# Optimization experiments

Measured on AMD Instinct MI355X. Metric: run time of the kernel, lower is better.

The kernel has to match this reference:

```python
import jax, jax.numpy as jnp
import numpy as np

IN_DIM = 64
OUT_DIM = 64
NUM_HEADS = 4
NEG_SLOPE = 0.2
GAMMA = 1.0  # constraint_gamma
NUM_VARS = 100000
NUM_CLAUSES = 100000
NUM_CLUSTERS = 2048
VARS_PER = 64
CLAUSES_PER = 64
NUM_EDGES = 400000


def _xavier(k, shape):
    bound = np.sqrt(6.0 / (shape[0] + shape[1])).astype(np.float32)
    return jax.random.uniform(k, shape, jnp.float32, -bound, bound)


def setup_inputs() -> dict:
    key = jax.random.key(0)
    ks = jax.random.split(key, 11)
    return {
        "x_var": jax.random.normal(ks[0], (NUM_VARS, IN_DIM), jnp.float32),
        "x_clause": jax.random.normal(ks[1], (NUM_CLAUSES, IN_DIM), jnp.float32),
        "var_clause_edge_index": jax.random.randint(ks[2], (2, NUM_EDGES), 0, NUM_VARS),
        "edge_polarity": jax.random.normal(ks[3], (NUM_EDGES, 1), jnp.float32),
        "cluster_var_ids": jax.random.randint(ks[4], (NUM_CLUSTERS, VARS_PER), 0, NUM_VARS),
        "cluster_clause_ids": jax.random.randint(ks[5], (NUM_CLUSTERS, CLAUSES_PER), 0, NUM_CLAUSES),
        "satisfaction_scores": jax.random.uniform(ks[6], (NUM_CLAUSES,), jnp.float32),
        "active_heads": 4,
        "W_Q": _xavier(ks[7], (OUT_DIM, IN_DIM)),
        "W_K": _xavier(ks[8], (OUT_DIM, IN_DIM)),
        "W_V": _xavier(ks[9], (OUT_DIM, IN_DIM)),
        "head_weights": jnp.ones((NUM_HEADS,), jnp.float32),
        "out_proj_w": _xavier(ks[10], (OUT_DIM, OUT_DIM)),
        "out_proj_b": jnp.zeros((OUT_DIM,), jnp.float32),
    }


def reference(x_var, x_clause, var_clause_edge_index, edge_polarity,
              cluster_var_ids, cluster_clause_ids, satisfaction_scores,
              active_heads, W_Q, W_K, W_V, head_weights, out_proj_w, out_proj_b):
    # NOTE: var_clause_edge_index / edge_polarity are accepted but unused,
    # matching the original forward body.
    num_vars = x_var.shape[0]
    x_all = jnp.concatenate([x_var, x_clause], axis=0)            # [N, D]
    Q = x_all @ W_Q.T
    K = x_all @ W_K.T
    V = x_all @ W_V.T

    # Block-diagonal cluster layout: [C, S] with S = VARS_PER + CLAUSES_PER
    nodes = jnp.concatenate([cluster_var_ids, cluster_clause_ids + num_vars], axis=1)
    Qc = Q[nodes]                                                 # [C, S, D]
    Kc = K[nodes]
    Vc = V[nodes]

    scale = jnp.asarray(np.sqrt(OUT_DIM), Qc.dtype)
    scores = jnp.einsum('csd,ctd->cst', Qc, Kc) / scale            # [C, S, S]
    # constraint-aware bias on clause columns (added before leaky_relu)
    bias = jnp.concatenate(
        [jnp.zeros(cluster_var_ids.shape, scores.dtype),
         GAMMA * satisfaction_scores[cluster_clause_ids]], axis=1)  # [C, S]
    scores = jax.nn.leaky_relu(scores + bias[:, None, :], NEG_SLOPE)
    attn = jax.nn.softmax(scores, axis=-1)

    head_w = jnp.mean(head_weights[:active_heads])
    h = jnp.einsum('cst,ctd->csd', attn, Vc) * head_w             # [C, S, D]

    flat = nodes.reshape(-1)
    out = jnp.zeros_like(x_all).at[flat].add(h.reshape(-1, OUT_DIM))
    count = jnp.zeros((x_all.shape[0],), x_all.dtype).at[flat].add(1.0)
    out = out / jnp.maximum(count, 1.0)[:, None]
    out = out @ out_proj_w.T + out_proj_b

    return (x_var + out[:num_vars], x_clause + out[num_vars:])
```

## Files before the change

kernel.cpp:

```cpp
#include <hip/hip_runtime.h>


#define NV 100000
#define NN 200000
#define NCLUST 2048
#define XS 72

typedef __attribute__((ext_vector_type(8))) short short8;
typedef __attribute__((ext_vector_type(16))) float floatx16;
typedef __attribute__((ext_vector_type(4))) unsigned uint4v;

__device__ __forceinline__ unsigned short f2bf(float f) {
    union { float f; unsigned u; } v; v.f = f;
    unsigned r = v.u + 0x7fffu + ((v.u >> 16) & 1u);
    return (unsigned short)(r >> 16);
}
__device__ __forceinline__ unsigned pack2bf(float lo, float hi) {
    union { float f; unsigned u; } a, b; a.f = lo; b.f = hi;
    unsigned ra = a.u + 0x7fffu + ((a.u >> 16) & 1u);
    unsigned rb = b.u + 0x7fffu + ((b.u >> 16) & 1u);
    return (ra >> 16) | (rb & 0xffff0000u);
}
__device__ __forceinline__ int crow(int r, int lane) {
    return (r & 3) + 8 * (r >> 2) + 4 * (lane >> 5);
}
__device__ __forceinline__ void bar_lds() {
    __builtin_amdgcn_sched_barrier(0);
    asm volatile("s_waitcnt lgkmcnt(0)" ::: "memory");
    __builtin_amdgcn_s_barrier();
    __builtin_amdgcn_sched_barrier(0);
}

#define ZU4 1650000
__global__ __launch_bounds__(256) void prep_kernel(
    const float* __restrict__ WQ, const float* __restrict__ WK,
    const float* __restrict__ WV, const float* __restrict__ Wout,
    const float* __restrict__ head_weights, const int* __restrict__ active_heads_p,
    unsigned short* __restrict__ Mtr, unsigned short* __restrict__ Pbf,
    uint4v* __restrict__ zbase)
{
    int o = blockIdx.x * blockDim.x + threadIdx.x;
    if (o < 4096) {
        int d = o >> 6, a = o & 63;
        float acc = 0.f;
        for (int j = 0; j < 64; ++j) acc += WQ[j*64 + a] * WK[j*64 + d];
        Mtr[o] = f2bf(acc * 0.125f);
    } else if (o < 8192) {
        int ah = active_heads_p[0];
        float hw = 0.f;
        for (int i = 0; i < ah; ++i) hw += head_weights[i];
        hw /= (float)ah;
        int o2 = o - 4096;
        int j = o2 >> 6, b = o2 & 63;
        float acc = 0.f;
        for (int d = 0; d < 64; ++d) acc += Wout[j*64 + d] * WV[d*64 + b];
        Pbf[o2] = f2bf(acc * hw);
    }
    uint4v z = {0u, 0u, 0u, 0u};
    for (int j = o; j < ZU4; j += 262144) zbase[j] = z;
}

template<bool WN>
__device__ __forceinline__ void cluster_compute(
    unsigned short* X, unsigned short* E,
    const int* ids, const float* biascl,
    const unsigned short* __restrict__ Mtr,
    unsigned short* __restrict__ accum_bf,
    int lane, int w, int m, int hk, int r, int cb,
    short8 nx0, short8 nx1, short8 nx2, short8 nx3)
{
    {
        floatx16 z0 = {}, z1 = {};
        #pragma unroll
        for (int ks = 0; ks < 4; ++ks) {
            short8 mb0 = *(const short8*)(Mtr + m * 64 + ks * 16 + hk);
            short8 mb1 = *(const short8*)(Mtr + (32 + m) * 64 + ks * 16 + hk);
            short8 a = *(const short8*)&X[(w * 32 + m) * XS + ks * 16 + hk];
            z0 = __builtin_amdgcn_mfma_f32_32x32x16_bf16(a, mb0, z0, 0, 0, 0);
            z1 = __builtin_amdgcn_mfma_f32_32x32x16_bf16(a, mb1, z1, 0, 0, 0);
        }
        #pragma unroll
        for (int rr = 0; rr < 16; ++rr) {
            int row = w * 32 + crow(rr, lane);
            E[row * XS + m]      = f2bf(z0[rr]);
            E[row * XS + 32 + m] = f2bf(z1[rr]);
        }
    }

    floatx16 sc[4] = {{}, {}, {}, {}};
    #pragma unroll
    for (int ks = 0; ks < 4; ++ks) {
        short8 a = *(const short8*)&E[(w * 32 + m) * XS + ks * 16 + hk];
        #pragma unroll
        for (int nt = 0; nt < 4; ++nt) {
            short8 b = *(const short8*)&X[(nt * 32 + m) * XS + ks * 16 + hk];
            sc[nt] = __builtin_amdgcn_mfma_f32_32x32x16_bf16(a, b, sc[nt], 0, 0, 0);
        }
    }

    const float b2 = biascl[m], b3 = biascl[32 + m];
    #pragma unroll
    for (int rr = 0; rr < 16; ++rr) {
        float a0 = sc[0][rr], a1 = sc[1][rr], a2 = sc[2][rr] + b2, a3 = sc[3][rr] + b3;
        a0 = a0 > 0.f ? a0 : 0.2f * a0;
        a1 = a1 > 0.f ? a1 : 0.2f * a1;
        a2 = a2 > 0.f ? a2 : 0.2f * a2;
        a3 = a3 > 0.f ? a3 : 0.2f * a3;
        a0 = __expf(a0); a1 = __expf(a1); a2 = __expf(a2); a3 = __expf(a3);
        float s4 = (a0 + a1) + (a2 + a3);
        #pragma unroll
        for (int off = 1; off < 32; off <<= 1) s4 += __shfl_xor(s4, off, 64);
        float inv = __builtin_amdgcn_rcpf(s4);
        sc[0][rr] = a0 * inv; sc[1][rr] = a1 * inv;
        sc[2][rr] = a2 * inv; sc[3][rr] = a3 * inv;
    }

    #pragma unroll
    for (int rr = 0; rr < 16; ++rr) {
        int row = w * 32 + crow(rr, lane);
        E[row * XS + m]      = f2bf(sc[0][rr]);
        E[row * XS + 32 + m] = f2bf(sc[1][rr]);
    }

    floatx16 g0 = {}, g1 = {};
    #pragma unroll
    for (int ks = 0; ks < 4; ++ks) {
        short8 a = *(const short8*)&E[(w * 32 + m) * XS + ks * 16 + hk];
        short8 b0, b1;
        #pragma unroll
        for (int j = 0; j < 8; ++j) {
            int t = ks * 16 + hk + j;
            b0[j] = (short)X[t * XS + m];
            b1[j] = (short)X[t * XS + 32 + m];
        }
        g0 = __builtin_amdgcn_mfma_f32_32x32x16_bf16(a, b0, g0, 0, 0, 0);
        g1 = __builtin_amdgcn_mfma_f32_32x32x16_bf16(a, b1, g1, 0, 0, 0);
    }

    #pragma unroll
    for (int rr = 0; rr < 16; ++rr) {
        int row = w * 32 + crow(rr, lane);
        E[row * XS + m]      = f2bf(sc[2][rr]);
        E[row * XS + 32 + m] = f2bf(sc[3][rr]);
    }

    #pragma unroll
    for (int ks = 0; ks < 4; ++ks) {
        short8 a = *(const short8*)&E[(w * 32 + m) * XS + ks * 16 + hk];
        short8 b0, b1;
        #pragma unroll
        for (int j = 0; j < 8; ++j) {
            int t = 64 + ks * 16 + hk + j;
            b0[j] = (short)X[t * XS + m];
            b1[j] = (short)X[t * XS + 32 + m];
        }
        g0 = __builtin_amdgcn_mfma_f32_32x32x16_bf16(a, b0, g0, 0, 0, 0);
        g1 = __builtin_amdgcn_mfma_f32_32x32x16_bf16(a, b1, g1, 0, 0, 0);
    }

    if (WN) {
        *(short8*)&E[r * XS + cb +  0] = nx0;
        *(short8*)&E[r * XS + cb +  8] = nx1;
        *(short8*)&E[r * XS + cb + 16] = nx2;
        *(short8*)&E[r * XS + cb + 24] = nx3;
    }

    const bool ev = !(lane & 1);
    const int colbase = ev ? m : (31 + m);
    #pragma unroll
    for (int rr = 0; rr < 16; ++rr) {
        int row = w * 32 + crow(rr, lane);
        int nid = ids[row];
        float a0 = g0[rr], a1 = g1[rr];
        float t0 = __shfl_xor(a0, 1, 64);
        float t1 = __shfl_xor(a1, 1, 64);
        float lo = ev ? a0 : t1;
        float hi = ev ? t0 : a1;
        unsigned pk = (unsigned)f2bf(lo) | ((unsigned)f2bf(hi) << 16);
        unsigned long long addr =
            (unsigned long long)(accum_bf + (size_t)nid * 64 + colbase);
        asm volatile("global_atomic_pk_add_bf16 %0, %1, off"
                     :: "v"(addr), "v"(pk) : "memory");
    }
}

__global__ __launch_bounds__(256, 4) void attn_kernel(
    const float* __restrict__ x_var, const float* __restrict__ x_clause,
    const int* __restrict__ cvar, const int* __restrict__ ccl,
    const float* __restrict__ sat, const unsigned short* __restrict__ Mtr,
    unsigned short* __restrict__ accum_bf, float* __restrict__ countv)
{
    __shared__ unsigned short bufA[128 * XS];
    __shared__ unsigned short bufB[128 * XS];
    __shared__ int   ids0[128], ids1[128];
    __shared__ float bias0[64], bias1[64];

    const int tid = threadIdx.x, lane = tid & 63, w = tid >> 6;
    const int m = lane & 31, hk = (lane >> 5) * 8;
    const int c0 = blockIdx.x * 2;
    const int r = tid >> 1, half = tid & 1, cb = half * 32;

    int nid0, nid1;
    const float *src0, *src1;
    float sv0 = 0.f, sv1 = 0.f;
    if (r < 64) {
        nid0 = cvar[c0 * 64 + r];
        nid1 = cvar[c0 * 64 + 64 + r];
        src0 = x_var + (size_t)nid0 * 64;
        src1 = x_var + (size_t)nid1 * 64;
    } else {
        int cid0 = ccl[c0 * 64 + (r - 64)];
        int cid1 = ccl[c0 * 64 + r];
        nid0 = NV + cid0; nid1 = NV + cid1;
        src0 = x_clause + (size_t)cid0 * 64;
        src1 = x_clause + (size_t)cid1 * 64;
        if (half) { sv0 = sat[cid0]; sv1 = sat[cid1]; }
    }

    const float4* s40 = (const float4*)src0 + half * 8;
    const float4* s41 = (const float4*)src1 + half * 8;
    float4 v0[8], v1[8];
    #pragma unroll
    for (int i = 0; i < 8; ++i) v0[i] = s40[i];
    #pragma unroll
    for (int i = 0; i < 8; ++i) v1[i] = s41[i];

    if (!half) {
        ids0[r] = nid0; ids1[r] = nid1;
        atomicAdd(&countv[nid0], 1.0f);
        atomicAdd(&countv[nid1], 1.0f);
    }
    if (r >= 64 && half) { bias0[r - 64] = sv0; bias1[r - 64] = sv1; }

    {
        union { unsigned u[16]; short8 v[4]; } h0;
        #pragma unroll
        for (int i = 0; i < 8; ++i) {
            h0.u[2*i]   = pack2bf(v0[i].x, v0[i].y);
            h0.u[2*i+1] = pack2bf(v0[i].z, v0[i].w);
        }
        #pragma unroll
        for (int i = 0; i < 4; ++i) *(short8*)&bufA[r * XS + cb + i * 8] = h0.v[i];
    }
    union { unsigned u[16]; short8 v[4]; } h1;
    #pragma unroll
    for (int i = 0; i < 8; ++i) {
        h1.u[2*i]   = pack2bf(v1[i].x, v1[i].y);
        h1.u[2*i+1] = pack2bf(v1[i].z, v1[i].w);
    }

    bar_lds();

    cluster_compute<true>(bufA, bufB, ids0, bias0, Mtr, accum_bf,
                          lane, w, m, hk, r, cb,
                          h1.v[0], h1.v[1], h1.v[2], h1.v[3]);

    bar_lds();

    short8 zz = {};
    cluster_compute<false>(bufB, bufA, ids1, bias1, Mtr, accum_bf,
                           lane, w, m, hk, r, cb, zz, zz, zz, zz);
}

__global__ __launch_bounds__(256, 4) void finalize_kernel(
    const float* __restrict__ x_var, const float* __restrict__ x_clause,
    const unsigned short* __restrict__ accum_bf, const float* __restrict__ countv,
    const unsigned short* __restrict__ Pbf, const float* __restrict__ bout,
    float* __restrict__ out)
{
    __shared__ float T[4][32][68];
    __shared__ float cnts[256];
    const int tid = threadIdx.x, lane = tid & 63, w = tid >> 6;
    const int base = blockIdx.x * 256;
    {
        int n = base + tid;
        cnts[tid] = (n < NN) ? countv[n] : 1.f;
    }
    __syncthreads();

    const int m = lane & 31, hk = (lane >> 5) * 8;
    short8 pb[2][4];
    #pragma unroll
    for (int nt = 0; nt < 2; ++nt)
        #pragma unroll
        for (int ks = 0; ks < 4; ++ks)
            pb[nt][ks] = *(const short8*)(Pbf + (nt * 32 + m) * 64 + ks * 16 + hk);
    const float bias0 = bout[m], bias1 = bout[32 + m];

    const int r2 = lane >> 1, cb2 = (lane & 1) * 32;

    #pragma unroll
    for (int tm = 0; tm < 2; ++tm) {
        int mt = w * 2 + tm;
        const unsigned short* arow = accum_bf + (size_t)(base + mt * 32 + m) * 64;
        floatx16 c0 = {}, c1 = {};
        #pragma unroll
        for (int ks = 0; ks < 4; ++ks) {
            short8 a = *(const short8*)(arow + ks * 16 + hk);
            c0 = __builtin_amdgcn_mfma_f32_32x32x16_bf16(a, pb[0][ks], c0, 0, 0, 0);
            c1 = __builtin_amdgcn_mfma_f32_32x32x16_bf16(a, pb[1][ks], c1, 0, 0, 0);
        }
        #pragma unroll
        for (int rr = 0; rr < 16; ++rr) {
            int lr32 = crow(rr, lane);
            float inv = 1.0f / fmaxf(cnts[mt * 32 + lr32], 1.0f);
            T[w][lr32][m]      = c0[rr] * inv + bias0;
            T[w][lr32][32 + m] = c1[rr] * inv + bias1;
        }
        int n2 = base + mt * 32 + r2;
        if (n2 < NN) {
            const float* xr = (n2 < NV) ? (x_var + (size_t)n2 * 64)
                                        : (x_clause + (size_t)(n2 - NV) * 64);
            float* orow = out + (size_t)n2 * 64;
            #pragma unroll
            for (int j = 0; j < 8; ++j) {
                float4 t = *(const float4*)&T[w][r2][cb2 + 4 * j];
                float4 xv = *(const float4*)&xr[cb2 + 4 * j];
                float4 o;
                o.x = t.x + xv.x; o.y = t.y + xv.y;
                o.z = t.z + xv.z; o.w = t.w + xv.w;
                *(float4*)&orow[cb2 + 4 * j] = o;
            }
        }
    }
}

extern "C" void kernel_launch(void* const* d_in, const int* in_sizes, int n_in,
                              void* d_out, int out_size, void* d_ws, size_t ws_size,
                              hipStream_t stream)
{
    const float* x_var        = (const float*)d_in[0];
    const float* x_clause     = (const float*)d_in[1];
    const int*   cvar         = (const int*)d_in[4];
    const int*   ccl          = (const int*)d_in[5];
    const float* sat          = (const float*)d_in[6];
    const int*   active_heads = (const int*)d_in[7];
    const float* WQ           = (const float*)d_in[8];
    const float* WK           = (const float*)d_in[9];
    const float* WV           = (const float*)d_in[10];
    const float* head_weights = (const float*)d_in[11];
    const float* Wout         = (const float*)d_in[12];
    const float* bout         = (const float*)d_in[13];

    unsigned short* accum_bf = (unsigned short*)d_ws;
    float* countv = (float*)(accum_bf + (size_t)NN * 64);
    unsigned short* Mtr = (unsigned short*)(countv + NN);
    unsigned short* Pbf = Mtr + 4096;

    prep_kernel<<<1024, 256, 0, stream>>>(WQ, WK, WV, Wout, head_weights,
                                          active_heads, Mtr, Pbf,
                                          (uint4v*)d_ws);
    attn_kernel<<<NCLUST / 2, 256, 0, stream>>>(
        x_var, x_clause, cvar, ccl, sat, Mtr, accum_bf, countv);
    finalize_kernel<<<(NN + 255) / 256, 256, 0, stream>>>(
        x_var, x_clause, accum_bf, countv, Pbf, bout, (float*)d_out);
}
```

Measured before the change: 209.7 us.

## Replace atomic bf16 scatter-add with CSR gather via count, scan and edge-id lists

Removes the global bf16 packed atomic scatter and float count atomics from the attention kernel. Each cluster's per-node outputs are now written densely to a staging buffer H, and a CSR index (counts, prefix-sum offsets, edge ids) is built in three small kernels. The finalize kernel then gathers and sums each node's rows before the projection. This eliminates atomic contention and the large zero-fill of the accumulator, at the cost of extra kernel launches, a 33 MB staging write and irregular per-lane gather loops in finalize.

Measured after the change: 239.0 us. 14.0% more time.

```diff
diff --git a/kernel.cpp b/kernel.cpp
--- a/kernel.cpp
+++ b/kernel.cpp
@@ -8,12 +8,14 @@
 
 typedef __attribute__((ext_vector_type(8))) short short8;
 typedef __attribute__((ext_vector_type(16))) float floatx16;
-typedef __attribute__((ext_vector_type(4))) unsigned uint4v;
 
 __device__ __forceinline__ unsigned short f2bf(float f) {
     union { float f; unsigned u; } v; v.f = f;
     unsigned r = v.u + 0x7fffu + ((v.u >> 16) & 1u);
     return (unsigned short)(r >> 16);
+}
+__device__ __forceinline__ float bf2f(unsigned short s) {
+    union { unsigned u; float f; } v; v.u = (unsigned)s << 16; return v.f;
 }
 __device__ __forceinline__ unsigned pack2bf(float lo, float hi) {
     union { float f; unsigned u; } a, b; a.f = lo; b.f = hi;
@@ -31,13 +33,13 @@
     __builtin_amdgcn_sched_barrier(0);
 }
 
-#define ZU4 1650000
-__global__ __launch_bounds__(256) void prep_kernel(
+__global__ __launch_bounds__(256) void prep_count_kernel(
     const float* __restrict__ WQ, const float* __restrict__ WK,
     const float* __restrict__ WV, const float* __restrict__ Wout,
     const float* __restrict__ head_weights, const int* __restrict__ active_heads_p,
+    const int* __restrict__ cvar, const int* __restrict__ ccl,
     unsigned short* __restrict__ Mtr, unsigned short* __restrict__ Pbf,
-    uint4v* __restrict__ zbase)
+    int* __restrict__ icnt)
 {
     int o = blockIdx.x * blockDim.x + threadIdx.x;
     if (o < 4096) {
@@ -56,16 +58,52 @@
         for (int d = 0; d < 64; ++d) acc += Wout[j*64 + d] * WV[d*64 + b];
         Pbf[o2] = f2bf(acc * hw);
     }
-    uint4v z = {0u, 0u, 0u, 0u};
-    for (int j = o; j < ZU4; j += 262144) zbase[j] = z;
+    int c = o >> 7, r = o & 127;
+    int nid = (r < 64) ? cvar[c * 64 + r] : (NV + ccl[c * 64 + (r - 64)]);
+    atomicAdd(&icnt[nid], 1);
+}
+
+__global__ __launch_bounds__(256) void scan_kernel(
+    const int* __restrict__ icnt, int* __restrict__ off,
+    int* __restrict__ cur, int* __restrict__ gbase)
+{
+    __shared__ int s[256];
+    __shared__ int sbase;
+    const int tid = threadIdx.x;
+    const int n = blockIdx.x * 256 + tid;
+    int c = (n < NN) ? icnt[n] : 0;
+    s[tid] = c;
+    __syncthreads();
+    #pragma unroll
+    for (int d = 1; d < 256; d <<= 1) {
+        int v = (tid >= d) ? s[tid - d] : 0;
+        __syncthreads();
+        s[tid] += v;
+        __syncthreads();
+    }
+    if (tid == 255) sbase = atomicAdd(gbase, s[255]);
+    __syncthreads();
+    int o = sbase + s[tid] - c;
+    if (n < NN) { off[n] = o; cur[n] = o; }
+}
+
+__global__ __launch_bounds__(256) void build_eids_kernel(
+    const int* __restrict__ cvar, const int* __restrict__ ccl,
+    int* __restrict__ cur, int* __restrict__ eids)
+{
+    int e = blockIdx.x * 256 + threadIdx.x;
+    int c = e >> 7, r = e & 127;
+    int nid = (r < 64) ? cvar[c * 64 + r] : (NV + ccl[c * 64 + (r - 64)]);
+    int slot = atomicAdd(&cur[nid], 1);
+    eids[slot] = e;
 }
 
 template<bool WN>
 __device__ __forceinline__ void cluster_compute(
     unsigned short* X, unsigned short* E,
-    const int* ids, const float* biascl,
+    const float* biascl,
     const unsigned short* __restrict__ Mtr,
-    unsigned short* __restrict__ accum_bf,
+    unsigned short* __restrict__ sbase,
     int lane, int w, int m, int hk, int r, int cb,
     short8 nx0, short8 nx1, short8 nx2, short8 nx3)
 {
@@ -170,17 +208,13 @@
     #pragma unroll
     for (int rr = 0; rr < 16; ++rr) {
         int row = w * 32 + crow(rr, lane);
-        int nid = ids[row];
         float a0 = g0[rr], a1 = g1[rr];
         float t0 = __shfl_xor(a0, 1, 64);
         float t1 = __shfl_xor(a1, 1, 64);
         float lo = ev ? a0 : t1;
         float hi = ev ? t0 : a1;
         unsigned pk = (unsigned)f2bf(lo) | ((unsigned)f2bf(hi) << 16);
-        unsigned long long addr =
-            (unsigned long long)(accum_bf + (size_t)nid * 64 + colbase);
-        asm volatile("global_atomic_pk_add_bf16 %0, %1, off"
-                     :: "v"(addr), "v"(pk) : "memory");
+        *(unsigned*)(sbase + (size_t)row * 64 + colbase) = pk;
     }
 }
 
@@ -188,11 +222,10 @@
     const float* __restrict__ x_var, const float* __restrict__ x_clause,
     const int* __restrict__ cvar, const int* __restrict__ ccl,
     const float* __restrict__ sat, const unsigned short* __restrict__ Mtr,
-    unsigned short* __restrict__ accum_bf, float* __restrict__ countv)
+    unsigned short* __restrict__ H)
 {
     __shared__ unsigned short bufA[128 * XS];
     __shared__ unsigned short bufB[128 * XS];
-    __shared__ int   ids0[128], ids1[128];
     __shared__ float bias0[64], bias1[64];
 
     const int tid = threadIdx.x, lane = tid & 63, w = tid >> 6;
@@ -200,18 +233,16 @@
     const int c0 = blockIdx.x * 2;
     const int r = tid >> 1, half = tid & 1, cb = half * 32;
 
-    int nid0, nid1;
     const float *src0, *src1;
     float sv0 = 0.f, sv1 = 0.f;
     if (r < 64) {
-        nid0 = cvar[c0 * 64 + r];
-        nid1 = cvar[c0 * 64 + 64 + r];
+        int nid0 = cvar[c0 * 64 + r];
+        int nid1 = cvar[c0 * 64 + 64 + r];
         src0 = x_var + (size_t)nid0 * 64;
         src1 = x_var + (size_t)nid1 * 64;
     } else {
         int cid0 = ccl[c0 * 64 + (r - 64)];
         int cid1 = ccl[c0 * 64 + r];
-        nid0 = NV + cid0; nid1 = NV + cid1;
         src0 = x_clause + (size_t)cid0 * 64;
         src1 = x_clause + (size_t)cid1 * 64;
         if (half) { sv0 = sat[cid0]; sv1 = sat[cid1]; }
@@ -225,11 +256,6 @@
     #pragma unroll
     for (int i = 0; i < 8; ++i) v1[i] = s41[i];
 
-    if (!half) {
-        ids0[r] = nid0; ids1[r] = nid1;
-        atomicAdd(&countv[nid0], 1.0f);
-        atomicAdd(&countv[nid1], 1.0f);
-    }
     if (r >= 64 && half) { bias0[r - 64] = sv0; bias1[r - 64] = sv1; }
 
     {
@@ -251,30 +277,36 @@
 
     bar_lds();
 
-    cluster_compute<true>(bufA, bufB, ids0, bias0, Mtr, accum_bf,
+    unsigned short* st0 = H + (size_t)c0 * 128 * 64;
+    unsigned short* st1 = st0 + 128 * 64;
+
+    cluster_compute<true>(bufA, bufB, bias0, Mtr, st0,
                           lane, w, m, hk, r, cb,
                           h1.v[0], h1.v[1], h1.v[2], h1.v[3]);
 
     bar_lds();
 
     short8 zz = {};
-    cluster_compute<false>(bufB, bufA, ids1, bias1, Mtr, accum_bf,
+    cluster_compute<false>(bufB, bufA, bias1, Mtr, st1,
                            lane, w, m, hk, r, cb, zz, zz, zz, zz);
 }
 
-__global__ __launch_bounds__(256, 4) void finalize_kernel(
+__global__ __launch_bounds__(256) void finalize_kernel(
     const float* __restrict__ x_var, const float* __restrict__ x_clause,
-    const unsigned short* __restrict__ accum_bf, const float* __restrict__ countv,
+    const unsigned short* __restrict__ H, const int* __restrict__ icnt,
+    const int* __restrict__ off, const int* __restrict__ eids,
     const unsigned short* __restrict__ Pbf, const float* __restrict__ bout,
     float* __restrict__ out)
 {
     __shared__ float T[4][32][68];
-    __shared__ float cnts[256];
+    __shared__ int scnt[128], soff[128];
     const int tid = threadIdx.x, lane = tid & 63, w = tid >> 6;
-    const int base = blockIdx.x * 256;
-    {
+    const int base = blockIdx.x * 128;
+    if (tid < 128) {
         int n = base + tid;
-        cnts[tid] = (n < NN) ? countv[n] : 1.f;
+        bool v = n < NN;
+        scnt[tid] = v ? icnt[n] : 0;
+        soff[tid] = v ? off[n] : 0;
     }
     __syncthreads();
 
@@ -287,40 +319,54 @@
             pb[nt][ks] = *(const short8*)(Pbf + (nt * 32 + m) * 64 + ks * 16 + hk);
     const float bias0 = bout[m], bias1 = bout[32 + m];
 
+    const int lr = w * 32 + m;
+    const int cc = scnt[lr];
+    const int o  = soff[lr];
+
+    float acc[4][8] = {};
+    for (int j = 0; j < cc; ++j) {
+        int e = eids[o + j];
+        const unsigned short* row = H + (size_t)e * 64;
+        #pragma unroll
+        for (int ks = 0; ks < 4; ++ks) {
+            short8 hv = *(const short8*)(row + ks * 16 + hk);
+            #pragma unroll
+            for (int q = 0; q < 8; ++q)
+                acc[ks][q] += bf2f((unsigned short)hv[q]);
+        }
+    }
+
+    floatx16 c0 = {}, c1 = {};
+    #pragma unroll
+    for (int ks = 0; ks < 4; ++ks) {
+        short8 a;
+        #pragma unroll
+        for (int q = 0; q < 8; ++q) a[q] = (short)f2bf(acc[ks][q]);
+        c0 = __builtin_amdgcn_mfma_f32_32x32x16_bf16(a, pb[0][ks], c0, 0, 0, 0);
+        c1 = __builtin_amdgcn_mfma_f32_32x32x16_bf16(a, pb[1][ks], c1, 0, 0, 0);
+    }
+
+    #pragma unroll
+    for (int rr = 0; rr < 16; ++rr) {
+        int lr32 = crow(rr, lane);
+        float inv = 1.0f / fmaxf((float)scnt[w * 32 + lr32], 1.0f);
+        T[w][lr32][m]      = c0[rr] * inv + bias0;
+        T[w][lr32][32 + m] = c1[rr] * inv + bias1;
+    }
     const int r2 = lane >> 1, cb2 = (lane & 1) * 32;
-
-    #pragma unroll
-    for (int tm = 0; tm < 2; ++tm) {
-        int mt = w * 2 + tm;
-        const unsigned short* arow = accum_bf + (size_t)(base + mt * 32 + m) * 64;
-        floatx16 c0 = {}, c1 = {};
-        #pragma unroll
-        for (int ks = 0; ks < 4; ++ks) {
-            short8 a = *(const short8*)(arow + ks * 16 + hk);
-            c0 = __builtin_amdgcn_mfma_f32_32x32x16_bf16(a, pb[0][ks], c0, 0, 0, 0);
-            c1 = __builtin_amdgcn_mfma_f32_32x32x16_bf16(a, pb[1][ks], c1, 0, 0, 0);
-        }
-        #pragma unroll
-        for (int rr = 0; rr < 16; ++rr) {
-            int lr32 = crow(rr, lane);
-            float inv = 1.0f / fmaxf(cnts[mt * 32 + lr32], 1.0f);
-            T[w][lr32][m]      = c0[rr] * inv + bias0;
-            T[w][lr32][32 + m] = c1[rr] * inv + bias1;
-        }
-        int n2 = base + mt * 32 + r2;
-        if (n2 < NN) {
-            const float* xr = (n2 < NV) ? (x_var + (size_t)n2 * 64)
-                                        : (x_clause + (size_t)(n2 - NV) * 64);
-            float* orow = out + (size_t)n2 * 64;
-            #pragma unroll
-            for (int j = 0; j < 8; ++j) {
-                float4 t = *(const float4*)&T[w][r2][cb2 + 4 * j];
-                float4 xv = *(const float4*)&xr[cb2 + 4 * j];
-                float4 o;
-                o.x = t.x + xv.x; o.y = t.y + xv.y;
-                o.z = t.z + xv.z; o.w = t.w + xv.w;
-                *(float4*)&orow[cb2 + 4 * j] = o;
-            }
+    int n2 = base + w * 32 + r2;
+    if (n2 < NN) {
+        const float* xr = (n2 < NV) ? (x_var + (size_t)n2 * 64)
+                                    : (x_clause + (size_t)(n2 - NV) * 64);
+        float* orow = out + (size_t)n2 * 64;
+        #pragma unroll
+        for (int j = 0; j < 8; ++j) {
+            float4 t = *(const float4*)&T[w][r2][cb2 + 4 * j];
+            float4 xv = *(const float4*)&xr[cb2 + 4 * j];
+            float4 ov;
+            ov.x = t.x + xv.x; ov.y = t.y + xv.y;
+            ov.z = t.z + xv.z; ov.w = t.w + xv.w;
+            *(float4*)&orow[cb2 + 4 * j] = ov;
         }
     }
 }
@@ -342,16 +388,30 @@
     const float* Wout         = (const float*)d_in[12];
     const float* bout         = (const float*)d_in[13];
 
-    unsigned short* accum_bf = (unsigned short*)d_ws;
-    float* countv = (float*)(accum_bf + (size_t)NN * 64);
-    unsigned short* Mtr = (unsigned short*)(countv + NN);
+    const size_t H_BYTES   = (size_t)NCLUST * 128 * 64 * 2;
+    const size_t ICNT_OFF  = H_BYTES;
+    const size_t GBASE_OFF = ICNT_OFF + (size_t)NN * 4;
+    const size_t OFF_OFF   = ICNT_OFF + 800256;
+    const size_t CUR_OFF   = OFF_OFF + 800256;
+    const size_t EIDS_OFF  = CUR_OFF + 800256;
+    const size_t MTR_OFF   = EIDS_OFF + (size_t)NCLUST * 128 * 4 + 256;
+
+    unsigned short* H   = (unsigned short*)d_ws;
+    int* icnt  = (int*)((char*)d_ws + ICNT_OFF);
+    int* gbase = (int*)((char*)d_ws + GBASE_OFF);
+    int* off   = (int*)((char*)d_ws + OFF_OFF);
+    int* cur   = (int*)((char*)d_ws + CUR_OFF);
+    int* eids  = (int*)((char*)d_ws + EIDS_OFF);
+    unsigned short* Mtr = (unsigned short*)((char*)d_ws + MTR_OFF);
     unsigned short* Pbf = Mtr + 4096;
 
-    prep_kernel<<<1024, 256, 0, stream>>>(WQ, WK, WV, Wout, head_weights,
-                                          active_heads, Mtr, Pbf,
-                                          (uint4v*)d_ws);
+    hipMemsetAsync(icnt, 0, (size_t)NN * 4 + 256, stream);
+    prep_count_kernel<<<1024, 256, 0, stream>>>(
+        WQ, WK, WV, Wout, head_weights, active_heads, cvar, ccl, Mtr, Pbf, icnt);
+    scan_kernel<<<(NN + 255) / 256, 256, 0, stream>>>(icnt, off, cur, gbase);
+    build_eids_kernel<<<1024, 256, 0, stream>>>(cvar, ccl, cur, eids);
     attn_kernel<<<NCLUST / 2, 256, 0, stream>>>(
-        x_var, x_clause, cvar, ccl, sat, Mtr, accum_bf, countv);
-    finalize_kernel<<<(NN + 255) / 256, 256, 0, stream>>>(
-        x_var, x_clause, accum_bf, countv, Pbf, bout, (float*)d_out);
-}
+        x_var, x_clause, cvar, ccl, sat, Mtr, H);
+    finalize_kernel<<<(NN + 127) / 128, 256, 0, stream>>>(
+        x_var, x_clause, H, icnt, off, eids, Pbf, bout, (float*)d_out);
+}
```
